# Kernel optimization log

Measured on AMD Instinct MI355X. Metric: run time of the kernel, lower is better.

Reference implementation:

```python
import jax, jax.numpy as jnp
import numpy as np

B, V = 128, 128256

def setup_inputs() -> dict:
    key = jax.random.key(0)
    k1, k2, k3, k4, k5 = jax.random.split(key, 5)
    logits = jax.random.normal(k1, (B, V), dtype=jnp.float32) * 2.0
    temperatures = jax.random.uniform(k2, (B,), dtype=jnp.float32) * 0.9 + 0.3  # [0.3, 1.2)
    top_ks = jax.random.randint(k3, (B,), 1, 65, dtype=jnp.int32)               # in [1, 64]
    top_ps = jax.random.uniform(k4, (B,), dtype=jnp.float32) * 0.85 + 0.1       # [0.1, 0.95)
    u = jax.random.uniform(k5, (B,), dtype=jnp.float32)                          # multinomial draw
    return {"logits": logits, "temperatures": temperatures, "top_ks": top_ks,
            "top_ps": top_ps, "u": u}

def reference(logits, temperatures, top_ks, top_ps, u):
    # logits /= temperatures ; probs = softmax(logits)
    probs = jax.nn.softmax(logits / temperatures[:, None], axis=-1)  # [B, V]
    # descending sort (argsort then gather so the permutation is explicit)
    idx = jnp.argsort(-probs, axis=-1)                               # [B, V] int
    probs_sort = jnp.take_along_axis(probs, idx, axis=-1)            # [B, V]
    probs_sum = jnp.cumsum(probs_sort, axis=-1)
    # top-p filter: zero where cumulative mass BEFORE this token exceeds top_p
    # top-k filter: zero beyond rank top_k
    ranks = jnp.arange(probs.shape[-1], dtype=jnp.int32)[None, :]
    mask = (probs_sum - probs_sort > top_ps[:, None]) | (ranks >= top_ks[:, None])
    probs_sort = jnp.where(mask, 0.0, probs_sort)
    # torch code divides by row max (multinomial renormalizes anyway)
    probs_sort = probs_sort / jnp.max(probs_sort, axis=-1, keepdims=True)
    # multinomial(num_samples=1) via inverse-CDF with one uniform per row
    cdf = jnp.cumsum(probs_sort, axis=-1)                            # [B, V]
    r = u[:, None] * cdf[:, -1:]
    sampled_rank = jnp.sum((cdf < r).astype(jnp.int32), axis=-1)     # [B]
    sampled_rank = jnp.clip(sampled_rank, 0, probs.shape[-1] - 1)
    batch_next_token_ids = jnp.take_along_axis(idx, sampled_rank[:, None], axis=-1)[:, 0]
    success = jnp.ones((probs.shape[0],), dtype=jnp.bool_)
    return batch_next_token_ids.astype(jnp.int32), success, probs_sort
```

## Files before the change

### kernel.cpp

```cpp
#include <hip/hip_runtime.h>
#include <math.h>

namespace {
constexpr int kB = 128;
constexpr int kV = 128256;
constexpr int kSplits = 16;
constexpr int kSplit = kV / kSplits;
constexpr int kSplit4 = kSplit / 4;
constexpr int kT1 = 256;
constexpr int kE = 8;
constexpr int kCap = 256;
constexpr int kTop = 64;

using f4v = __attribute__((ext_vector_type(4))) float;

__device__ __forceinline__ unsigned fkey(float y) {
  unsigned u = __float_as_uint(y);
  return ((int)u < 0) ? ~u : (u | 0x80000000u);
}
__device__ __forceinline__ float keyinv(unsigned k) {
  unsigned u = (k & 0x80000000u) ? (k & 0x7fffffffu) : ~k;
  return __uint_as_float(u);
}

__device__ __forceinline__ void bar_lds() {
  __builtin_amdgcn_sched_barrier(0);
  asm volatile("s_waitcnt lgkmcnt(0)" ::: "memory");
  __builtin_amdgcn_s_barrier();
  __builtin_amdgcn_sched_barrier(0);
}

__device__ __forceinline__ unsigned long long merge_desc(
    unsigned long long v, unsigned long long b, int lane) {
  v = v > b ? v : b;
#pragma unroll
  for (int j = 32; j; j >>= 1) {
    unsigned long long o = __shfl_xor(v, j);
    v = ((lane & j) == 0) ? (v > o ? v : o) : (v < o ? v : o);
  }
  return v;
}

__global__ __launch_bounds__(kT1) void k_select(
    const float* __restrict__ logits, const float* __restrict__ temps,
    float* __restrict__ out,
    float* __restrict__ wm, float* __restrict__ wS,
    unsigned long long* __restrict__ wpk) {
  const int sp = blockIdx.x, row = blockIdx.y, tid = threadIdx.x;
  const int lane = tid & 63, wid = tid >> 6;
  __shared__ float wred[4];
  __shared__ float ssum[4];
  __shared__ int cnt2[2][4];
  __shared__ unsigned long long cand[kCap];
  __shared__ int scnt;

  if (tid == 0) scnt = 0;
  const float t = temps[row];
  const float invt = 1.0f / t;
  const size_t rowbase = (size_t)row * kV + (size_t)sp * kSplit;
  const float4* in4 = (const float4*)(logits + rowbase);
  f4v* out4 = (f4v*)(out + 2 * kB + rowbase);
  const float nI = -INFINITY;

  float4 r[kE];
  float m = nI;
#pragma unroll
  for (int e = 0; e < kE; ++e) {
    int f = tid + e * kT1;
    float4 l;
    if (f < kSplit4) l = in4[f];
    else l = make_float4(nI, nI, nI, nI);
    r[e] = l;
    m = fmaxf(m, fmaxf(fmaxf(l.x, l.y), fmaxf(l.z, l.w)));
  }
  for (int o = 32; o; o >>= 1) m = fmaxf(m, __shfl_xor(m, o));
  if (lane == 0) wred[wid] = m;
  bar_lds();
  const float M = fmaxf(fmaxf(wred[0], wred[1]), fmaxf(wred[2], wred[3]));
  const float My = M / t;
  const float negMy = -My;

  {
    const f4v z4 = {0.f, 0.f, 0.f, 0.f};
#pragma unroll
    for (int e = 0; e < kE; ++e) {
      int f = tid + e * kT1;
      if (f < kSplit4) __builtin_nontemporal_store(z4, out4 + f);
    }
  }

  float s = 0.f;
#pragma unroll
  for (int e = 0; e < kE; ++e) {
    s += __expf(fmaf(r[e].x, invt, negMy));
    s += __expf(fmaf(r[e].y, invt, negMy));
    s += __expf(fmaf(r[e].z, invt, negMy));
    s += __expf(fmaf(r[e].w, invt, negMy));
  }
  for (int o = 32; o; o >>= 1) s += __shfl_xor(s, o);
  if (lane == 0) ssum[wid] = s;
  bar_lds();
  const float Ssp = ssum[0] + ssum[1] + ssum[2] + ssum[3];

  unsigned lo = 0x00800000u;
  unsigned hi = fkey(M) + 1;
  for (int it = 0; it < 32 && hi - lo > 1; ++it) {
    unsigned mid = lo + ((hi - lo) >> 1);
    if (it == 0) {
      unsigned p0 = fkey(M - 3.0f);
      if (p0 > lo && p0 < hi) mid = p0;
    } else if (it == 1) {
      unsigned p1 = fkey(M - 4.5f);
      if (p1 > lo && p1 < hi) mid = p1;
    }
    const float mf = keyinv(mid);
    int cw = 0;
#pragma unroll
    for (int e = 0; e < kE; ++e) {
      cw += (int)__popcll(__ballot(r[e].x >= mf));
      cw += (int)__popcll(__ballot(r[e].y >= mf));
      cw += (int)__popcll(__ballot(r[e].z >= mf));
      cw += (int)__popcll(__ballot(r[e].w >= mf));
    }
    if (lane == 0) cnt2[it & 1][wid] = cw;
    bar_lds();
    const int c = cnt2[it & 1][0] + cnt2[it & 1][1] +
                  cnt2[it & 1][2] + cnt2[it & 1][3];
    if (c >= kTop) { lo = mid; if (c <= kCap) break; }
    else hi = mid;
  }
  const float Tf = keyinv(lo);

#pragma unroll
  for (int e = 0; e < kE; ++e) {
    int f = tid + e * kT1;
    const float vals[4] = {r[e].x, r[e].y, r[e].z, r[e].w};
#pragma unroll
    for (int j = 0; j < 4; ++j) {
      const float lv = vals[j];
      if (lv >= Tf) {
        int pos = atomicAdd(&scnt, 1);
        if (pos < kCap)
          cand[pos] = ((unsigned long long)fkey(lv) << 32) |
                      (unsigned)~(unsigned)(sp * kSplit + f * 4 + j);
      }
    }
  }
  bar_lds();
  const int nc = scnt < kCap ? scnt : kCap;
  unsigned long long v = (tid < nc) ? cand[tid] : 0ULL;

  for (int k2 = 2; k2 <= 64; k2 <<= 1) {
    for (int j = k2 >> 1; j; j >>= 1) {
      unsigned long long o = __shfl_xor(v, j);
      const bool keep_max = (((lane & k2) == 0) == ((lane & j) == 0));
      v = keep_max ? (o > v ? o : v) : (o < v ? o : v);
    }
  }
  cand[tid] = v;
  bar_lds();
  if (wid == 0) {
    v = cand[lane];
#pragma unroll
    for (int s2 = 1; s2 < 4; ++s2)
      v = merge_desc(v, cand[s2 * 64 + (63 - lane)], lane);
    wpk[((size_t)row * kSplits + sp) * kTop + lane] = v;
    if (lane == 0) {
      wm[row * kSplits + sp] = My;
      wS[row * kSplits + sp] = Ssp;
    }
  }
}

__global__ __launch_bounds__(kT1) void k_sample(
    const float* __restrict__ temps,
    const int* __restrict__ top_ks, const float* __restrict__ top_ps,
    const float* __restrict__ uin,
    const float* __restrict__ wm, const float* __restrict__ wS,
    const unsigned long long* __restrict__ wpk, float* __restrict__ out) {
  const int row = blockIdx.x, tid = threadIdx.x;
  const int lane = tid & 63, wid = tid >> 6;
  __shared__ unsigned long long runs[kT1];
  __shared__ float mArr[kSplits], sArr[kSplits];

  if (tid >= kT1 - kSplits) {
    const int s2 = tid - (kT1 - kSplits);
    mArr[s2] = wm[row * kSplits + s2];
    sArr[s2] = wS[row * kSplits + s2];
  }
  const unsigned long long* basek = wpk + (size_t)row * (kSplits * kTop);
  unsigned long long mv = basek[(size_t)(4 * wid) * kTop + lane];
#pragma unroll
  for (int s2 = 1; s2 < 4; ++s2) {
    unsigned long long b = basek[(size_t)(4 * wid + s2) * kTop + (kTop - 1 - lane)];
    mv = merge_desc(mv, b, lane);
  }
  runs[tid] = mv;
  __syncthreads();
  if (wid != 0) return;

  mv = runs[lane];
#pragma unroll
  for (int s2 = 1; s2 < 4; ++s2)
    mv = merge_desc(mv, runs[s2 * 64 + (63 - lane)], lane);
  const float tvl = keyinv((unsigned)(mv >> 32)) / temps[row];
  const int til = (int)(~(unsigned)(mv & 0xffffffffu));

  float MM = -INFINITY;
  for (int s2 = 0; s2 < kSplits; ++s2) MM = fmaxf(MM, mArr[s2]);
  float SS = 0.f;
  for (int s2 = 0; s2 < kSplits; ++s2)
    SS += expf(mArr[s2] - MM) * sArr[s2];

  const float tp = top_ps[row];
  const int kk = top_ks[row];
  const float uu = uin[row];

  float cum = 0.f, q0 = 0.f, qa_keep = 0.f;
  for (int r2 = 0; r2 < kTop; ++r2) {
    const float tvr = __shfl(tvl, r2);
    const float pr = expf(tvr - MM) / SS;
    cum += pr;
    const float cb = cum - pr;
    const float q = ((cb > tp) || (r2 >= kk)) ? 0.f : pr;
    if (r2 == 0) q0 = q;
    if (lane == r2) qa_keep = q;
  }
  float tot = 0.f, sv_keep = 0.f, cdf_keep = 0.f;
  for (int r2 = 0; r2 < kTop; ++r2) {
    const float qr = __shfl(qa_keep, r2);
    const float sr = qr / q0;
    tot += sr;
    if (lane == r2) { sv_keep = sr; cdf_keep = tot; }
  }
  const float rth = uu * tot;
  int cnt = (int)__popcll(__ballot(cdf_keep < rth));
  if (cnt > kTop - 1) cnt = kTop - 1;
  const int sampled = __shfl(til, cnt);

  if (lane == 0) {
    out[row] = (float)sampled;
    out[kB + row] = 1.0f;
  }
  out[2 * kB + (size_t)row * kV + lane] = sv_keep;
}
}

extern "C" void kernel_launch(void* const* d_in, const int* in_sizes, int n_in,
                              void* d_out, int out_size, void* d_ws, size_t ws_size,
                              hipStream_t stream) {
  const float* logits = (const float*)d_in[0];
  const float* temps  = (const float*)d_in[1];
  const int*   top_ks = (const int*)d_in[2];
  const float* top_ps = (const float*)d_in[3];
  const float* uin    = (const float*)d_in[4];
  float* out = (float*)d_out;

  float* wm = (float*)d_ws;
  float* wS = wm + kB * kSplits;
  unsigned long long* wpk =
      (unsigned long long*)(wS + kB * kSplits + kB * kSplits);

  k_select<<<dim3(kSplits, kB), kT1, 0, stream>>>(logits, temps, out, wm, wS, wpk);
  k_sample<<<kB, kT1, 0, stream>>>(temps, top_ks, top_ps, uin, wm, wS, wpk, out);
}
```

Before: 48.63 us.

## Split selection into single-wave blocks with ballot compaction and no barriers

```diff
diff --git a/kernel.cpp b/kernel.cpp
--- a/kernel.cpp
+++ b/kernel.cpp
@@ -4,13 +4,14 @@
 namespace {
 constexpr int kB = 128;
 constexpr int kV = 128256;
-constexpr int kSplits = 16;
+constexpr int kSplits = 64;
 constexpr int kSplit = kV / kSplits;
 constexpr int kSplit4 = kSplit / 4;
-constexpr int kT1 = 256;
+constexpr int kW = 64;
 constexpr int kE = 8;
-constexpr int kCap = 256;
+constexpr int kCap = 128;
 constexpr int kTop = 64;
+constexpr int kT2 = 256;
 
 using f4v = __attribute__((ext_vector_type(4))) float;
 
@@ -23,10 +24,9 @@
   return __uint_as_float(u);
 }
 
-__device__ __forceinline__ void bar_lds() {
+__device__ __forceinline__ void wave_lds_fence() {
   __builtin_amdgcn_sched_barrier(0);
   asm volatile("s_waitcnt lgkmcnt(0)" ::: "memory");
-  __builtin_amdgcn_s_barrier();
   __builtin_amdgcn_sched_barrier(0);
 }
 
@@ -41,20 +41,29 @@
   return v;
 }
 
-__global__ __launch_bounds__(kT1) void k_select(
+__device__ __forceinline__ unsigned long long sort64_desc(
+    unsigned long long v, int lane) {
+#pragma unroll
+  for (int k2 = 2; k2 <= 64; k2 <<= 1) {
+#pragma unroll
+    for (int j = k2 >> 1; j; j >>= 1) {
+      unsigned long long o = __shfl_xor(v, j);
+      const bool keep_max = (((lane & k2) == 0) == ((lane & j) == 0));
+      v = keep_max ? (o > v ? o : v) : (o < v ? o : v);
+    }
+  }
+  return v;
+}
+
+__global__ __launch_bounds__(kW) void k_select(
     const float* __restrict__ logits, const float* __restrict__ temps,
     float* __restrict__ out,
     float* __restrict__ wm, float* __restrict__ wS,
     unsigned long long* __restrict__ wpk) {
-  const int sp = blockIdx.x, row = blockIdx.y, tid = threadIdx.x;
-  const int lane = tid & 63, wid = tid >> 6;
-  __shared__ float wred[4];
-  __shared__ float ssum[4];
-  __shared__ int cnt2[2][4];
+  const int sp = blockIdx.x, row = blockIdx.y;
+  const int lane = threadIdx.x;
   __shared__ unsigned long long cand[kCap];
-  __shared__ int scnt;
-
-  if (tid == 0) scnt = 0;
+
   const float t = temps[row];
   const float invt = 1.0f / t;
   const size_t rowbase = (size_t)row * kV + (size_t)sp * kSplit;
@@ -66,7 +75,7 @@
   float m = nI;
 #pragma unroll
   for (int e = 0; e < kE; ++e) {
-    int f = tid + e * kT1;
+    int f = lane + e * kW;
     float4 l;
     if (f < kSplit4) l = in4[f];
     else l = make_float4(nI, nI, nI, nI);
@@ -74,9 +83,7 @@
     m = fmaxf(m, fmaxf(fmaxf(l.x, l.y), fmaxf(l.z, l.w)));
   }
   for (int o = 32; o; o >>= 1) m = fmaxf(m, __shfl_xor(m, o));
-  if (lane == 0) wred[wid] = m;
-  bar_lds();
-  const float M = fmaxf(fmaxf(wred[0], wred[1]), fmaxf(wred[2], wred[3]));
+  const float M = m;
   const float My = M / t;
   const float negMy = -My;
 
@@ -84,7 +91,7 @@
     const f4v z4 = {0.f, 0.f, 0.f, 0.f};
 #pragma unroll
     for (int e = 0; e < kE; ++e) {
-      int f = tid + e * kT1;
+      int f = lane + e * kW;
       if (f < kSplit4) __builtin_nontemporal_store(z4, out4 + f);
     }
   }
@@ -98,9 +105,7 @@
     s += __expf(fmaf(r[e].w, invt, negMy));
   }
   for (int o = 32; o; o >>= 1) s += __shfl_xor(s, o);
-  if (lane == 0) ssum[wid] = s;
-  bar_lds();
-  const float Ssp = ssum[0] + ssum[1] + ssum[2] + ssum[3];
+  const float Ssp = s;
 
   unsigned lo = 0x00800000u;
   unsigned hi = fkey(M) + 1;
@@ -110,69 +115,62 @@
       unsigned p0 = fkey(M - 3.0f);
       if (p0 > lo && p0 < hi) mid = p0;
     } else if (it == 1) {
-      unsigned p1 = fkey(M - 4.5f);
+      unsigned p1 = fkey(M - 4.0f);
       if (p1 > lo && p1 < hi) mid = p1;
     }
     const float mf = keyinv(mid);
-    int cw = 0;
+    int c = 0;
 #pragma unroll
     for (int e = 0; e < kE; ++e) {
-      cw += (int)__popcll(__ballot(r[e].x >= mf));
-      cw += (int)__popcll(__ballot(r[e].y >= mf));
-      cw += (int)__popcll(__ballot(r[e].z >= mf));
-      cw += (int)__popcll(__ballot(r[e].w >= mf));
-    }
-    if (lane == 0) cnt2[it & 1][wid] = cw;
-    bar_lds();
-    const int c = cnt2[it & 1][0] + cnt2[it & 1][1] +
-                  cnt2[it & 1][2] + cnt2[it & 1][3];
+      c += (int)__popcll(__ballot(r[e].x >= mf));
+      c += (int)__popcll(__ballot(r[e].y >= mf));
+      c += (int)__popcll(__ballot(r[e].z >= mf));
+      c += (int)__popcll(__ballot(r[e].w >= mf));
+    }
     if (c >= kTop) { lo = mid; if (c <= kCap) break; }
     else hi = mid;
   }
   const float Tf = keyinv(lo);
 
+  const unsigned long long lmask = (1ULL << lane) - 1ULL;
+  int base = 0;
 #pragma unroll
   for (int e = 0; e < kE; ++e) {
-    int f = tid + e * kT1;
+    int f = lane + e * kW;
     const float vals[4] = {r[e].x, r[e].y, r[e].z, r[e].w};
 #pragma unroll
     for (int j = 0; j < 4; ++j) {
       const float lv = vals[j];
-      if (lv >= Tf) {
-        int pos = atomicAdd(&scnt, 1);
+      const bool p = lv >= Tf;
+      const unsigned long long mk = __ballot(p);
+      if (p) {
+        const int pos = base + (int)__popcll(mk & lmask);
         if (pos < kCap)
           cand[pos] = ((unsigned long long)fkey(lv) << 32) |
                       (unsigned)~(unsigned)(sp * kSplit + f * 4 + j);
       }
-    }
-  }
-  bar_lds();
-  const int nc = scnt < kCap ? scnt : kCap;
-  unsigned long long v = (tid < nc) ? cand[tid] : 0ULL;
-
-  for (int k2 = 2; k2 <= 64; k2 <<= 1) {
-    for (int j = k2 >> 1; j; j >>= 1) {
-      unsigned long long o = __shfl_xor(v, j);
-      const bool keep_max = (((lane & k2) == 0) == ((lane & j) == 0));
-      v = keep_max ? (o > v ? o : v) : (o < v ? o : v);
-    }
-  }
-  cand[tid] = v;
-  bar_lds();
-  if (wid == 0) {
-    v = cand[lane];
-#pragma unroll
-    for (int s2 = 1; s2 < 4; ++s2)
-      v = merge_desc(v, cand[s2 * 64 + (63 - lane)], lane);
-    wpk[((size_t)row * kSplits + sp) * kTop + lane] = v;
-    if (lane == 0) {
-      wm[row * kSplits + sp] = My;
-      wS[row * kSplits + sp] = Ssp;
-    }
-  }
-}
-
-__global__ __launch_bounds__(kT1) void k_sample(
+      base += (int)__popcll(mk);
+    }
+  }
+  const int nc = base < kCap ? base : kCap;
+  if (lane >= nc) cand[lane] = 0ULL;
+  if (kW + lane >= nc) cand[kW + lane] = 0ULL;
+  wave_lds_fence();
+  unsigned long long v0 = cand[lane];
+  unsigned long long v1 = cand[kW + lane];
+
+  v0 = sort64_desc(v0, lane);
+  v1 = sort64_desc(v1, lane);
+  v0 = merge_desc(v0, __shfl(v1, 63 - lane), lane);
+
+  wpk[((size_t)row * kSplits + sp) * kTop + lane] = v0;
+  if (lane == 0) {
+    wm[row * kSplits + sp] = My;
+    wS[row * kSplits + sp] = Ssp;
+  }
+}
+
+__global__ __launch_bounds__(kT2) void k_sample(
     const float* __restrict__ temps,
     const int* __restrict__ top_ks, const float* __restrict__ top_ps,
     const float* __restrict__ uin,
@@ -180,19 +178,19 @@
     const unsigned long long* __restrict__ wpk, float* __restrict__ out) {
   const int row = blockIdx.x, tid = threadIdx.x;
   const int lane = tid & 63, wid = tid >> 6;
-  __shared__ unsigned long long runs[kT1];
+  __shared__ unsigned long long runs[kT2];
   __shared__ float mArr[kSplits], sArr[kSplits];
 
-  if (tid >= kT1 - kSplits) {
-    const int s2 = tid - (kT1 - kSplits);
-    mArr[s2] = wm[row * kSplits + s2];
-    sArr[s2] = wS[row * kSplits + s2];
+  if (wid == 3) {
+    mArr[lane] = wm[row * kSplits + lane];
+    sArr[lane] = wS[row * kSplits + lane];
   }
   const unsigned long long* basek = wpk + (size_t)row * (kSplits * kTop);
-  unsigned long long mv = basek[(size_t)(4 * wid) * kTop + lane];
-#pragma unroll
-  for (int s2 = 1; s2 < 4; ++s2) {
-    unsigned long long b = basek[(size_t)(4 * wid + s2) * kTop + (kTop - 1 - lane)];
+  unsigned long long mv = basek[(size_t)(16 * wid) * kTop + lane];
+#pragma unroll
+  for (int s2 = 1; s2 < 16; ++s2) {
+    unsigned long long b =
+        basek[(size_t)(16 * wid + s2) * kTop + (kTop - 1 - lane)];
     mv = merge_desc(mv, b, lane);
   }
   runs[tid] = mv;
@@ -261,6 +259,6 @@
   unsigned long long* wpk =
       (unsigned long long*)(wS + kB * kSplits + kB * kSplits);
 
-  k_select<<<dim3(kSplits, kB), kT1, 0, stream>>>(logits, temps, out, wm, wS, wpk);
-  k_sample<<<kB, kT1, 0, stream>>>(temps, top_ks, top_ps, uin, wm, wS, wpk, out);
-}
+  k_select<<<dim3(kSplits, kB), kW, 0, stream>>>(logits, temps, out, wm, wS, wpk);
+  k_sample<<<kB, kT2, 0, stream>>>(temps, top_ks, top_ps, uin, wm, wS, wpk, out);
+}
```

After: 56.44 us. +16.1%, slower.
